# Performance work log

Measured on AMD Instinct MI355X. Metric: run time of the kernel, lower is better.

Reference implementation:

```python
import jax, jax.numpy as jnp
import numpy as np

NUM_BANKS = 32  # bank size (num_heads in __init__)
D_HEAD = 128
D_MODEL = 2048
B, S, K = 2, 1024, 4  # batch, seq, selected heads per token


def setup_inputs() -> dict:
    key = jax.random.key(0)
    k1, k2, k3, k4, k5 = jax.random.split(key, 5)
    tensor = jax.random.normal(k1, (B, S, K, D_HEAD), dtype=jnp.float32)
    head_selection = jax.random.randint(k2, (B, S, K), 0, NUM_BANKS)
    head_probabilities = jax.random.uniform(k3, (B, S, K), dtype=jnp.float32)
    # Banked linear parameters: one (d_head, d_model) matrix + bias per bank.
    W = jax.random.normal(k4, (NUM_BANKS, D_HEAD, D_MODEL), dtype=jnp.float32) * (1.0 / np.sqrt(D_HEAD))
    b = jax.random.normal(k5, (NUM_BANKS, D_MODEL), dtype=jnp.float32) * 0.01
    return {"tensor": tensor, "head_selection": head_selection,
            "head_probabilities": head_probabilities, "W": W, "b": b}


def reference(tensor, head_selection, head_probabilities, W, b):
    # BankedLinear: per (token, head-slot) select weight matrix W[sel] and
    # compute x @ W[sel] + b[sel] -> (..., k, d_model).
    # Implemented as a one-hot dispatch so the contraction is a single
    # grouped-GEMM-shaped einsum instead of materializing an
    # (B,S,K,d_head,d_model) gathered weight tensor.
    onehot = jax.nn.one_hot(head_selection, NUM_BANKS, dtype=tensor.dtype)  # (B,S,K,N)
    proj = jnp.einsum('bskd,bskn,ndm->bskm', tensor, onehot, W)             # (B,S,K,d_model)
    proj = proj + jnp.einsum('bskn,nm->bskm', onehot, b)                    # gathered bias
    # Head merge: matmul(proj^T, probs.unsqueeze(-1)).squeeze(-1)
    # == probability-weighted sum over the head dimension.
    out = jnp.einsum('bskm,bsk->bsm', proj, head_probabilities)             # (B,S,d_model)
    return out
```

## Files before the change

kernel.cpp:

```cpp
#include <hip/hip_runtime.h>
#include <hip/hip_bf16.h>

#define NBANK 32
#define DHEAD 128
#define DMODEL 2048
#define NSLOT 8192
#define NTOK 2048
#define XCROWS 1024
#define CONV_BLOCKS 4096

typedef __attribute__((ext_vector_type(8))) short short8;
typedef __attribute__((ext_vector_type(8))) float float8;
typedef __attribute__((ext_vector_type(4))) float f32x4;

__device__ __forceinline__ unsigned short f2bf(float f) {
    union { __hip_bfloat16 h; unsigned short u; } cvt;
    cvt.h = __float2bfloat16(f);
    return cvt.u;
}
__device__ __forceinline__ float bf2f(unsigned short u) {
    union { float f; unsigned int v; } cvt;
    cvt.v = ((unsigned int)u) << 16;
    return cvt.f;
}

__global__ void prep_kernel(const float* __restrict__ W,
                            unsigned short* __restrict__ wfrag,
                            const int* __restrict__ sel,
                            int* __restrict__ counts,
                            int* __restrict__ lists) {
    if (blockIdx.x < CONV_BLOCKS) {
        int t = blockIdx.x * 256 + threadIdx.x;
        int lane = t & 63;
        int kk = (t >> 6) & 3;
        int mt = (t >> 8) & 127;
        int bank = t >> 15;
        int m = mt * 16 + (lane & 15);
        int kbase = kk * 32 + (lane >> 4) * 8;
        const float* src = W + ((size_t)bank * DHEAD + kbase) * DMODEL + m;
        short8 o;
        #pragma unroll
        for (int v = 0; v < 8; ++v)
            o[v] = (short)f2bf(src[v * DMODEL]);
        reinterpret_cast<short8*>(wfrag)[t] = o;
    } else {
        __shared__ int lcount[NBANK];
        __shared__ int lbase[NBANK];
        int tid = threadIdx.x;
        int slot = (blockIdx.x - CONV_BLOCKS) * 256 + tid;
        if (tid < NBANK) lcount[tid] = 0;
        __syncthreads();
        int bank = sel[slot];
        int mypos = atomicAdd(&lcount[bank], 1);
        __syncthreads();
        if (tid < NBANK) lbase[tid] = atomicAdd(&counts[tid], lcount[tid]);
        __syncthreads();
        lists[bank * NSLOT + lbase[bank] + mypos] = slot;
    }
}

__global__ void compact_kernel(const float* __restrict__ x,
                               const float* __restrict__ probs,
                               const int* __restrict__ counts,
                               const int* __restrict__ lists,
                               unsigned short* __restrict__ xc) {
    int bank = blockIdx.x;
    int wv = (threadIdx.x >> 6) + blockIdx.y * 4;
    int lane = threadIdx.x & 63;
    int cnt = min(counts[bank], XCROWS);
    for (int pos = wv; pos < cnt; pos += 16) {
        int slot = lists[bank * NSLOT + pos];
        float p = probs[slot];
        float2 v = reinterpret_cast<const float2*>(x + (size_t)slot * DHEAD)[lane];
        ushort2 o;
        o.x = f2bf(v.x * p);
        o.y = f2bf(v.y * p);
        reinterpret_cast<ushort2*>(xc + ((size_t)bank * XCROWS + pos) * DHEAD)[lane] = o;
    }
}

__global__ __launch_bounds__(256, 4)
void gemm_kernel(const unsigned short* __restrict__ wfrag,
                 const unsigned short* __restrict__ xc,
                 const int* __restrict__ counts,
                 const int* __restrict__ lists,
                 unsigned short* __restrict__ proj) {
    __shared__ __align__(16) unsigned short A_lds[16 * DHEAD];
    __shared__ int slots_lds[16];

    int tid = threadIdx.x;
    int w = tid >> 6;
    int lane = tid & 63;
    int lane_lo = lane & 15;
    int lane_hi = lane >> 4;
    int bank = blockIdx.y;
    int mw = blockIdx.x * 128 + w * 32;
    int mt0 = mw >> 4;
    int cnt = min(counts[bank], XCROWS);

    const short8* wf = reinterpret_cast<const short8*>(wfrag);
    short8 bw[4][2];
    #pragma unroll
    for (int nf = 0; nf < 2; ++nf)
        #pragma unroll
        for (int kk = 0; kk < 4; ++kk)
            bw[kk][nf] = wf[((((bank * 128 + mt0 + nf) * 4) + kk) << 6) + lane];

    int row16 = tid >> 4, j = tid & 15;
    const char* xc_b = reinterpret_cast<const char*>(xc)
                     + ((size_t)bank * XCROWS + row16) * 256
                     + ((j ^ (row16 & 7)) << 4);
    char* lds_b = reinterpret_cast<char*>(A_lds);
    char* lds_dst = lds_b + (w << 10);

    for (int rt = blockIdx.z; rt * 16 < cnt; rt += 2) {
        __syncthreads();
        __builtin_amdgcn_global_load_lds(
            (const __attribute__((address_space(1))) void*)(xc_b + (size_t)rt * 4096),
            (__attribute__((address_space(3))) void*)lds_dst, 16, 0, 0);
        if (tid < 16) {
            int ridx = rt * 16 + tid;
            slots_lds[tid] = (ridx < cnt) ? lists[bank * NSLOT + ridx] : -1;
        }
        __syncthreads();

        f32x4 acc0 = {0.f, 0.f, 0.f, 0.f};
        f32x4 acc1 = {0.f, 0.f, 0.f, 0.f};
        #pragma unroll
        for (int kk = 0; kk < 4; ++kk) {
            int byteoff = lane_lo * 256 +
                          ((kk * 64 + lane_hi * 16) ^ ((lane_lo & 7) << 4));
            short8 a = *reinterpret_cast<const short8*>(lds_b + byteoff);
            acc0 = __builtin_amdgcn_mfma_f32_16x16x32_bf16(a, bw[kk][0], acc0, 0, 0, 0);
            acc1 = __builtin_amdgcn_mfma_f32_16x16x32_bf16(a, bw[kk][1], acc1, 0, 0, 0);
        }

        #pragma unroll
        for (int v = 0; v < 4; ++v) {
            int row = lane_hi * 4 + v;
            int slot = slots_lds[row];
            if (slot >= 0) {
                unsigned short* pr = proj + (size_t)slot * DMODEL + mw + lane_lo;
                pr[0]  = f2bf(acc0[v]);
                pr[16] = f2bf(acc1[v]);
            }
        }
    }
}

__global__ void merge_kernel(const unsigned short* __restrict__ proj,
                             const int* __restrict__ sel,
                             const float* __restrict__ probs,
                             const float* __restrict__ bias,
                             float* __restrict__ out) {
    int tid = threadIdx.x;
    int tok = blockIdx.x;
    float8 acc = {0.f, 0.f, 0.f, 0.f, 0.f, 0.f, 0.f, 0.f};
    #pragma unroll
    for (int k = 0; k < 4; ++k) {
        int slot = tok * 4 + k;
        short8 pr = reinterpret_cast<const short8*>(proj + (size_t)slot * DMODEL)[tid];
        float p = probs[slot];
        int bk = sel[slot];
        float8 bv = reinterpret_cast<const float8*>(bias + (size_t)bk * DMODEL)[tid];
        #pragma unroll
        for (int jj = 0; jj < 8; ++jj)
            acc[jj] += bf2f((unsigned short)pr[jj]) + p * bv[jj];
    }
    reinterpret_cast<float8*>(out + (size_t)tok * DMODEL)[tid] = acc;
}

extern "C" void kernel_launch(void* const* d_in, const int* in_sizes, int n_in,
                              void* d_out, int out_size, void* d_ws, size_t ws_size,
                              hipStream_t stream) {
    const float* x     = (const float*)d_in[0];
    const int*   sel   = (const int*)  d_in[1];
    const float* probs = (const float*)d_in[2];
    const float* W     = (const float*)d_in[3];
    const float* bias  = (const float*)d_in[4];
    float* out = (float*)d_out;

    char* ws = (char*)d_ws;
    int* counts = (int*)ws;
    int* lists  = (int*)(ws + 1024);
    unsigned short* xc    = (unsigned short*)(ws + (3u  << 20));
    unsigned short* wfrag = (unsigned short*)(ws + (12u << 20));
    unsigned short* proj  = (unsigned short*)(ws + (32u << 20));

    hipMemsetAsync(counts, 0, 128, stream);
    prep_kernel<<<CONV_BLOCKS + 32, 256, 0, stream>>>(W, wfrag, sel, counts, lists);
    compact_kernel<<<dim3(32, 4), 256, 0, stream>>>(x, probs, counts, lists, xc);
    gemm_kernel<<<dim3(16, 32, 2), 256, 0, stream>>>(wfrag, xc, counts, lists, proj);
    merge_kernel<<<2048, 256, 0, stream>>>(proj, sel, probs, bias, out);
}
```

Measured before the change: 128.7 us.

## Fuse bank bucketing and row compaction into prep kernel, drop memset and z-split

Each of the 32 bucketing blocks now owns one bank. It scans all 8192 selections, builds a deterministic list with a block-wide prefix sum, writes its count, and then compacts and scales the x rows into bf16 itself. This removes the memset, the global atomics and the separate compact launch. The GEMM grid also drops its z=2 row-tile split, so each block loops over all row tiles of its bank. The trade-off is that each bucketing block rereads the full selection array and the compaction runs on only 32 blocks, while the GEMM has half as many blocks, which reduces parallelism.

After: 157.1 us. 22.1% more time.

```diff
diff --git a/kernel.cpp b/kernel.cpp
--- a/kernel.cpp
+++ b/kernel.cpp
@@ -27,8 +27,11 @@
 __global__ void prep_kernel(const float* __restrict__ W,
                             unsigned short* __restrict__ wfrag,
                             const int* __restrict__ sel,
+                            const float* __restrict__ x,
+                            const float* __restrict__ probs,
                             int* __restrict__ counts,
-                            int* __restrict__ lists) {
+                            int* __restrict__ lists,
+                            unsigned short* __restrict__ xc) {
     if (blockIdx.x < CONV_BLOCKS) {
         int t = blockIdx.x * 256 + threadIdx.x;
         int lane = t & 63;
@@ -44,38 +47,38 @@
             o[v] = (short)f2bf(src[v * DMODEL]);
         reinterpret_cast<short8*>(wfrag)[t] = o;
     } else {
-        __shared__ int lcount[NBANK];
-        __shared__ int lbase[NBANK];
+        int b = blockIdx.x - CONV_BLOCKS;
         int tid = threadIdx.x;
-        int slot = (blockIdx.x - CONV_BLOCKS) * 256 + tid;
-        if (tid < NBANK) lcount[tid] = 0;
+        __shared__ int sc[256];
+        int base0 = tid * 32;
+        int c = 0;
+        for (int i = 0; i < 32; ++i) c += (sel[base0 + i] == b) ? 1 : 0;
+        sc[tid] = c;
         __syncthreads();
-        int bank = sel[slot];
-        int mypos = atomicAdd(&lcount[bank], 1);
+        for (int off = 1; off < 256; off <<= 1) {
+            int v = (tid >= off) ? sc[tid - off] : 0;
+            __syncthreads();
+            sc[tid] += v;
+            __syncthreads();
+        }
+        int pos = sc[tid] - c;
+        for (int i = 0; i < 32; ++i) {
+            int slot = base0 + i;
+            if (sel[slot] == b) lists[b * NSLOT + pos++] = slot;
+        }
+        if (tid == 255) counts[b] = sc[255];
         __syncthreads();
-        if (tid < NBANK) lbase[tid] = atomicAdd(&counts[tid], lcount[tid]);
-        __syncthreads();
-        lists[bank * NSLOT + lbase[bank] + mypos] = slot;
-    }
-}
-
-__global__ void compact_kernel(const float* __restrict__ x,
-                               const float* __restrict__ probs,
-                               const int* __restrict__ counts,
-                               const int* __restrict__ lists,
-                               unsigned short* __restrict__ xc) {
-    int bank = blockIdx.x;
-    int wv = (threadIdx.x >> 6) + blockIdx.y * 4;
-    int lane = threadIdx.x & 63;
-    int cnt = min(counts[bank], XCROWS);
-    for (int pos = wv; pos < cnt; pos += 16) {
-        int slot = lists[bank * NSLOT + pos];
-        float p = probs[slot];
-        float2 v = reinterpret_cast<const float2*>(x + (size_t)slot * DHEAD)[lane];
-        ushort2 o;
-        o.x = f2bf(v.x * p);
-        o.y = f2bf(v.y * p);
-        reinterpret_cast<ushort2*>(xc + ((size_t)bank * XCROWS + pos) * DHEAD)[lane] = o;
+        int wv = tid >> 6, lane = tid & 63;
+        int cnt = min(sc[255], XCROWS);
+        for (int p = wv; p < cnt; p += 4) {
+            int slot = lists[b * NSLOT + p];
+            float pr = probs[slot];
+            float2 v2 = reinterpret_cast<const float2*>(x + (size_t)slot * DHEAD)[lane];
+            ushort2 o;
+            o.x = f2bf(v2.x * pr);
+            o.y = f2bf(v2.y * pr);
+            reinterpret_cast<ushort2*>(xc + ((size_t)b * XCROWS + p) * DHEAD)[lane] = o;
+        }
     }
 }
 
@@ -113,7 +116,7 @@
     char* lds_b = reinterpret_cast<char*>(A_lds);
     char* lds_dst = lds_b + (w << 10);
 
-    for (int rt = blockIdx.z; rt * 16 < cnt; rt += 2) {
+    for (int rt = 0; rt * 16 < cnt; ++rt) {
         __syncthreads();
         __builtin_amdgcn_global_load_lds(
             (const __attribute__((address_space(1))) void*)(xc_b + (size_t)rt * 4096),
@@ -187,9 +190,8 @@
     unsigned short* wfrag = (unsigned short*)(ws + (12u << 20));
     unsigned short* proj  = (unsigned short*)(ws + (32u << 20));
 
-    hipMemsetAsync(counts, 0, 128, stream);
-    prep_kernel<<<CONV_BLOCKS + 32, 256, 0, stream>>>(W, wfrag, sel, counts, lists);
-    compact_kernel<<<dim3(32, 4), 256, 0, stream>>>(x, probs, counts, lists, xc);
-    gemm_kernel<<<dim3(16, 32, 2), 256, 0, stream>>>(wfrag, xc, counts, lists, proj);
+    prep_kernel<<<CONV_BLOCKS + 32, 256, 0, stream>>>(W, wfrag, sel, x, probs,
+                                                      counts, lists, xc);
+    gemm_kernel<<<dim3(16, 32), 256, 0, stream>>>(wfrag, xc, counts, lists, proj);
     merge_kernel<<<2048, 256, 0, stream>>>(proj, sel, probs, bias, out);
 }
```
